# Performance work log

Measured on AMD Instinct MI355X. Metric: run time of the kernel, lower is better.

The kernel has to match this reference:

```python
import jax, jax.numpy as jnp
import numpy as np

DIM = 1024
MEM = 512
HEAD = DIM // 2


def setup_inputs() -> dict:
    key = jax.random.key(0)
    k0, k1, k2, k3, k4 = jax.random.split(key, 5)
    x = jax.random.normal(k0, (4, 8192, DIM), dtype=jnp.float32)
    keys_real = jax.random.normal(k1, (MEM, HEAD), dtype=jnp.float32) * 0.02
    keys_imag = jax.random.normal(k2, (MEM, HEAD), dtype=jnp.float32) * 0.02
    values_real = jax.random.normal(k3, (MEM, HEAD), dtype=jnp.float32) * 0.02
    values_imag = jax.random.normal(k4, (MEM, HEAD), dtype=jnp.float32) * 0.02
    return {"x": x, "keys_real": keys_real, "keys_imag": keys_imag,
            "values_real": values_real, "values_imag": values_imag}


def reference(x, keys_real, keys_imag, values_real, values_imag):
    input_shape = x.shape
    temperature = HEAD ** (-0.5)
    x_flat = x.reshape(-1, DIM)                       # [N, dim]
    q, p = jnp.split(x_flat, 2, axis=-1)              # each [N, head]
    # dual real/imag score matmuls summed -> energy [N, mem]
    energy = jnp.einsum('nh,mh->nm', q, keys_real) + jnp.einsum('nh,mh->nm', p, keys_imag)
    attn = jax.nn.softmax(energy * temperature, axis=-1)
    out_real = jnp.einsum('nm,mh->nh', attn, values_real)
    out_imag = jnp.einsum('nm,mh->nh', attn, values_imag)
    return jnp.concatenate([out_real, out_imag], axis=-1).reshape(input_shape)
```

## Files before the change

kernel.cpp:

```cpp
#include <hip/hip_runtime.h>


#define DIMX   1024
#define MEMN   512
#define NROWS  32768
#define TEMP   0.04419417382415922f

typedef __bf16 bf16;
typedef __bf16 bf16x8 __attribute__((ext_vector_type(8)));
typedef float  f32x4  __attribute__((ext_vector_type(4)));

__device__ __forceinline__ void gload_lds16(const void* g, void* l) {
    __builtin_amdgcn_global_load_lds(
        (const __attribute__((address_space(1))) unsigned*)g,
        (__attribute__((address_space(3))) unsigned*)l,
        16, 0, 0);
}
__device__ __forceinline__ void gl_b16x8(bf16x8& d, const bf16* p) {
    asm volatile("global_load_dwordx4 %0, %1, off" : "=v"(d) : "v"(p));
}
__device__ __forceinline__ void gl_f32x4(f32x4& d, const float* p) {
    asm volatile("global_load_dwordx4 %0, %1, off" : "=v"(d) : "v"(p));
}
#define VMW(N)     do { asm volatile("s_waitcnt vmcnt(" #N ")" ::: "memory"); \
                        __builtin_amdgcn_sched_barrier(0); } while (0)
#define WAITBAR(N) do { asm volatile("s_waitcnt vmcnt(" #N ") lgkmcnt(0)\n\t" \
                        "s_barrier" ::: "memory");                            \
                        __builtin_amdgcn_sched_barrier(0); } while (0)
#define VMWBAR(N)  do { asm volatile("s_waitcnt vmcnt(" #N ")\n\t"            \
                        "s_barrier" ::: "memory");                            \
                        __builtin_amdgcn_sched_barrier(0); } while (0)

__global__ __launch_bounds__(256) void pack_kv_kernel(const float* __restrict__ kr,
                                                      const float* __restrict__ ki,
                                                      const float* __restrict__ vr,
                                                      const float* __restrict__ vi,
                                                      bf16* __restrict__ Kb,
                                                      bf16* __restrict__ Vb) {
    const int idx = blockIdx.x * 256 + threadIdx.x;
    const int e = idx & 7, l = (idx >> 3) & 63;
    const int lm = l & 15, g = l >> 4;
    {
        const int t = (idx >> 9) & 31, c = idx >> 14;
        const int row = t * 16 + lm, k = c * 32 + g * 8 + e;
        const float v = (k < 512) ? kr[row * 512 + k] : ki[row * 512 + (k - 512)];
        Kb[idx] = (bf16)v;
    }
    {
        const int t = (idx >> 9) & 63, c = idx >> 15;
        const int h = t * 16 + lm, m = c * 32 + g * 8 + e;
        const float v = (h < 512) ? vr[m * 512 + h] : vi[m * 512 + (h - 512)];
        Vb[idx] = (bf16)v;
    }
}

__global__ __launch_bounds__(256, 2) void energy_softmax_kernel(
        const float* __restrict__ x,
        const bf16*  __restrict__ Kb,
        bf16* __restrict__ attn) {
    __shared__ __align__(16) bf16 Xs[2][64 * 32];
    __shared__ float red[64][4][2];

    const int tid  = threadIdx.x;
    const int wv   = tid >> 6, lane = tid & 63;
    const int lm   = lane & 15, g = lane >> 4;
    const int rowB = blockIdx.x * 64;

    const int sr = tid >> 2, sc = tid & 3;
    const float* xsrc = x + (size_t)(rowB + sr) * DIMX + sc * 8;
    const int xw_off = sr * 64 + ((sc ^ ((sr >> 1) & 3)) << 4);

    const bf16* kbase = Kb + (wv * 8) * 512 + lane * 8;

    f32x4 acc[4][8] = {};
    f32x4 xa, xb;
    bf16x8 kf0[8], kf1[8];

#define K_PREF(DST, C) { _Pragma("unroll") for (int j = 0; j < 8; ++j)         \
        gl_b16x8(DST[j], kbase + (size_t)(C) * 16384 + j * 512); }
#define X_PREF(S) { gl_f32x4(xa, xsrc + (S) * 32);                             \
                    gl_f32x4(xb, xsrc + (S) * 32 + 4); }
#define X_WR(B) { bf16x8 w;                                                    \
    w[0]=(bf16)xa[0]; w[1]=(bf16)xa[1]; w[2]=(bf16)xa[2]; w[3]=(bf16)xa[3];    \
    w[4]=(bf16)xb[0]; w[5]=(bf16)xb[1]; w[6]=(bf16)xb[2]; w[7]=(bf16)xb[3];    \
    *(bf16x8*)((char*)Xs[B] + xw_off) = w; }
#define COMPUTE_E(XB, KF) { bf16x8 af[4];                                      \
    _Pragma("unroll") for (int i = 0; i < 4; ++i) { const int r = i * 16 + lm; \
        af[i] = *(const bf16x8*)((const char*)Xs[XB] + r * 64                  \
                                 + ((g ^ ((r >> 1) & 3)) << 4)); }             \
    __builtin_amdgcn_s_setprio(1);                                             \
    _Pragma("unroll") for (int i = 0; i < 4; ++i)                              \
        _Pragma("unroll") for (int j = 0; j < 8; ++j)                          \
            acc[i][j] = __builtin_amdgcn_mfma_f32_16x16x32_bf16(               \
                af[i], KF[j], acc[i][j], 0, 0, 0);                             \
    __builtin_amdgcn_s_setprio(0); }
#define STEP_E(KCUR, KNXT, XB, CH_K, CH_X)                                     \
    K_PREF(KNXT, CH_K);                                   \
    VMW(10);                              \
    COMPUTE_E(XB, KCUR);                                                       \
    VMW(8);                                                 \
    X_WR((XB) ^ 1);                                                           \
    X_PREF(CH_X);                                         \
    WAITBAR(10);

    X_PREF(0);
    K_PREF(kf0, 0);
    VMW(8);  X_WR(0);
    X_PREF(1);
    WAITBAR(10);

    for (int t = 0; t < 30; t += 2) {
        STEP_E(kf0, kf1, 0, t + 1, t + 2);
        STEP_E(kf1, kf0, 1, t + 2, t + 3);
    }
    K_PREF(kf1, 31);
    VMW(10);
    COMPUTE_E(0, kf0);
    VMW(8);
    X_WR(1);
    WAITBAR(8);
    VMW(0);
    COMPUTE_E(1, kf1);

#undef K_PREF
#undef X_PREF
#undef X_WR
#undef COMPUTE_E
#undef STEP_E

    float fac[4][4];
    #pragma unroll
    for (int i = 0; i < 4; ++i) {
        #pragma unroll
        for (int rg = 0; rg < 4; ++rg) {
            float m = acc[i][0][rg] * TEMP;
            #pragma unroll
            for (int j = 1; j < 8; ++j) m = fmaxf(m, acc[i][j][rg] * TEMP);
            m = fmaxf(m, __shfl_xor(m, 1));
            m = fmaxf(m, __shfl_xor(m, 2));
            m = fmaxf(m, __shfl_xor(m, 4));
            m = fmaxf(m, __shfl_xor(m, 8));
            float s = 0.f;
            #pragma unroll
            for (int j = 0; j < 8; ++j) {
                const float v = __expf(acc[i][j][rg] * TEMP - m);
                acc[i][j][rg] = v;
                s += v;
            }
            s += __shfl_xor(s, 1);
            s += __shfl_xor(s, 2);
            s += __shfl_xor(s, 4);
            s += __shfl_xor(s, 8);
            const int rr = i * 16 + g * 4 + rg;
            if (lm == 0) { red[rr][wv][0] = m; red[rr][wv][1] = s; }
            fac[i][rg] = m;
        }
    }
    __syncthreads();
    #pragma unroll
    for (int i = 0; i < 4; ++i) {
        #pragma unroll
        for (int rg = 0; rg < 4; ++rg) {
            const int rr = i * 16 + g * 4 + rg;
            const float m0 = red[rr][0][0], s0 = red[rr][0][1];
            const float m1 = red[rr][1][0], s1 = red[rr][1][1];
            const float m2 = red[rr][2][0], s2 = red[rr][2][1];
            const float m3 = red[rr][3][0], s3 = red[rr][3][1];
            const float M  = fmaxf(fmaxf(m0, m1), fmaxf(m2, m3));
            const float S  = s0 * __expf(m0 - M) + s1 * __expf(m1 - M)
                           + s2 * __expf(m2 - M) + s3 * __expf(m3 - M);
            fac[i][rg] = __expf(fac[i][rg] - M) / S;
        }
    }
    #pragma unroll
    for (int i = 0; i < 4; ++i) {
        #pragma unroll
        for (int rg = 0; rg < 4; ++rg) {
            const size_t rr = (size_t)(rowB + i * 16 + g * 4 + rg);
            bf16* p = attn + rr * MEMN + wv * 128 + lm;
            const float f = fac[i][rg];
            #pragma unroll
            for (int j = 0; j < 8; ++j)
                p[j * 16] = (bf16)(acc[i][j][rg] * f);
        }
    }
}

__global__ __launch_bounds__(256, 2) void gemm2_kernel(const bf16* __restrict__ A,
                                                       const bf16* __restrict__ Vb,
                                                       float* __restrict__ C) {
    __shared__ __align__(16) bf16 As[4][128 * 32];

    const int cpx = gridDim.x >> 3;
    const int l   = ((int)blockIdx.x & 7) * cpx + ((int)blockIdx.x >> 3);
    const int bx  = l & 7, by = l >> 3;

    const int tid  = threadIdx.x;
    const int wave = tid >> 6, lane = tid & 63;
    const int lm   = lane & 15, g = lane >> 4;
    const int rowB = by * 128;
    const int wrow = (wave >> 1) * 64;

    const bf16* vbase = Vb + (bx * 8 + (wave & 1) * 4) * 512 + lane * 8;

    f32x4 acc[4][4] = {};
    bf16x8 bf0[4], bf1[4];

#define A_STAGE(BI, C0) { _Pragma("unroll") for (int li = 0; li < 2; ++li) {    \
        const int q = wave * 2 + li;                                            \
        const int r = q * 16 + (lane >> 2);                                     \
        const int ch = lane & 3;                                                \
        gload_lds16(A + (size_t)(rowB + r) * 512 + (C0) * 32                    \
                      + ((ch ^ ((r >> 1) & 3)) << 3),                           \
                    (char*)As[BI] + q * 1024); } }
#define B_PREF(DST, C0) { _Pragma("unroll") for (int j = 0; j < 4; ++j)         \
        gl_b16x8(DST[j], vbase + (size_t)(C0) * 32768 + j * 512); }
#define COMPUTE_G(BI, BF) { bf16x8 af[4];                                       \
    _Pragma("unroll") for (int i = 0; i < 4; ++i) {                             \
        const int r = wrow + i * 16 + lm;                                       \
        af[i] = *(const bf16x8*)((const char*)As[BI] + r * 64                   \
                                 + ((g ^ ((r >> 1) & 3)) << 4)); }              \
    __builtin_amdgcn_s_setprio(1);                                              \
    _Pragma("unroll") for (int i = 0; i < 4; ++i)                               \
        _Pragma("unroll") for (int j = 0; j < 4; ++j)                           \
            acc[i][j] = __builtin_amdgcn_mfma_f32_16x16x32_bf16(                \
                af[i], BF[j], acc[i][j], 0, 0, 0);                              \
    __builtin_amdgcn_s_setprio(0); }
#define STEP_G(BCUR, BNXT, T)                                                   \
    A_STAGE((T + 2) & 3, T + 2);                     \
    B_PREF(BNXT, T + 1);                                             \
    VMW(6);                             \
    VMWBAR(6);                        \
    COMPUTE_G((T) & 3, BCUR);

    A_STAGE(0, 0);
    A_STAGE(1, 1);
    B_PREF(bf0, 0);
    for (int t = 0; t < 14; t += 2) {
        STEP_G(bf0, bf1, t);
        STEP_G(bf1, bf0, t + 1);
    }
    B_PREF(bf1, 15);
    VMW(4);
    VMWBAR(4);
    COMPUTE_G(2, bf0);
    VMW(0);
    COMPUTE_G(3, bf1);

#undef A_STAGE
#undef B_PREF
#undef COMPUTE_G
#undef STEP_G

    const int r0 = rowB + wrow + g * 4;
    const int c0 = bx * 128 + (wave & 1) * 64 + lm;
    #pragma unroll
    for (int i = 0; i < 4; ++i) {
        #pragma unroll
        for (int j = 0; j < 4; ++j) {
            #pragma unroll
            for (int r = 0; r < 4; ++r)
                C[(size_t)(r0 + i * 16 + r) * DIMX + (c0 + j * 16)] = acc[i][j][r];
        }
    }
}

extern "C" void kernel_launch(void* const* d_in, const int* in_sizes, int n_in,
                              void* d_out, int out_size, void* d_ws, size_t ws_size,
                              hipStream_t stream) {
    const float* x  = (const float*)d_in[0];
    const float* kr = (const float*)d_in[1];
    const float* ki = (const float*)d_in[2];
    const float* vr = (const float*)d_in[3];
    const float* vi = (const float*)d_in[4];
    float* out = (float*)d_out;

    char* ws = (char*)d_ws;
    bf16* Kb   = (bf16*)ws;
    bf16* Vb   = (bf16*)(ws + 1048576);
    bf16* attn = (bf16*)(ws + 2097152);

    pack_kv_kernel<<<2048, 256, 0, stream>>>(kr, ki, vr, vi, Kb, Vb);
    energy_softmax_kernel<<<512, 256, 0, stream>>>(x, Kb, attn);
    gemm2_kernel<<<2048, 256, 0, stream>>>(attn, Vb, out);
}
```

Measured before the change: 291.5 us.

## Enlarge both kernels to 512-thread blocks with wider row and column tiles

The energy/softmax kernel now runs 8 waves per block over 128 rows, each wave covering 64 memory columns, so each staged X tile is reused across more keys. The cross-wave softmax reduction widens to 8 partials. The second GEMM now uses 512-thread blocks covering 128 rows by 512 output columns, with each wave owning a 64-column strip and all 128 rows, which reduces re-reads of the attention matrix. The cost is more accumulator registers per thread, which can cut occupancy, and the vmcnt waits were retuned by hand to match the new load counts.

```diff
diff --git a/kernel.cpp b/kernel.cpp
--- a/kernel.cpp
+++ b/kernel.cpp
@@ -54,29 +54,29 @@
     }
 }
 
-__global__ __launch_bounds__(256, 2) void energy_softmax_kernel(
+__global__ __launch_bounds__(512, 2) void energy_softmax_kernel(
         const float* __restrict__ x,
         const bf16*  __restrict__ Kb,
         bf16* __restrict__ attn) {
-    __shared__ __align__(16) bf16 Xs[2][64 * 32];
-    __shared__ float red[64][4][2];
+    __shared__ __align__(16) bf16 Xs[2][128 * 32];
+    __shared__ float red[128][8][2];
 
     const int tid  = threadIdx.x;
     const int wv   = tid >> 6, lane = tid & 63;
     const int lm   = lane & 15, g = lane >> 4;
-    const int rowB = blockIdx.x * 64;
+    const int rowB = blockIdx.x * 128;
 
     const int sr = tid >> 2, sc = tid & 3;
     const float* xsrc = x + (size_t)(rowB + sr) * DIMX + sc * 8;
     const int xw_off = sr * 64 + ((sc ^ ((sr >> 1) & 3)) << 4);
 
-    const bf16* kbase = Kb + (wv * 8) * 512 + lane * 8;
-
-    f32x4 acc[4][8] = {};
+    const bf16* kbase = Kb + (wv * 4) * 512 + lane * 8;
+
+    f32x4 acc[8][4] = {};
     f32x4 xa, xb;
-    bf16x8 kf0[8], kf1[8];
-
-#define K_PREF(DST, C) { _Pragma("unroll") for (int j = 0; j < 8; ++j)         \
+    bf16x8 kf0[4], kf1[4];
+
+#define K_PREF(DST, C) { _Pragma("unroll") for (int j = 0; j < 4; ++j)         \
         gl_b16x8(DST[j], kbase + (size_t)(C) * 16384 + j * 512); }
 #define X_PREF(S) { gl_f32x4(xa, xsrc + (S) * 32);                             \
                     gl_f32x4(xb, xsrc + (S) * 32 + 4); }
@@ -84,41 +84,41 @@
     w[0]=(bf16)xa[0]; w[1]=(bf16)xa[1]; w[2]=(bf16)xa[2]; w[3]=(bf16)xa[3];    \
     w[4]=(bf16)xb[0]; w[5]=(bf16)xb[1]; w[6]=(bf16)xb[2]; w[7]=(bf16)xb[3];    \
     *(bf16x8*)((char*)Xs[B] + xw_off) = w; }
-#define COMPUTE_E(XB, KF) { bf16x8 af[4];                                      \
-    _Pragma("unroll") for (int i = 0; i < 4; ++i) { const int r = i * 16 + lm; \
+#define COMPUTE_E(XB, KF) { bf16x8 af[8];                                      \
+    _Pragma("unroll") for (int i = 0; i < 8; ++i) { const int r = i * 16 + lm; \
         af[i] = *(const bf16x8*)((const char*)Xs[XB] + r * 64                  \
                                  + ((g ^ ((r >> 1) & 3)) << 4)); }             \
     __builtin_amdgcn_s_setprio(1);                                             \
-    _Pragma("unroll") for (int i = 0; i < 4; ++i)                              \
-        _Pragma("unroll") for (int j = 0; j < 8; ++j)                          \
+    _Pragma("unroll") for (int i = 0; i < 8; ++i)                              \
+        _Pragma("unroll") for (int j = 0; j < 4; ++j)                          \
             acc[i][j] = __builtin_amdgcn_mfma_f32_16x16x32_bf16(               \
                 af[i], KF[j], acc[i][j], 0, 0, 0);                             \
     __builtin_amdgcn_s_setprio(0); }
 #define STEP_E(KCUR, KNXT, XB, CH_K, CH_X)                                     \
     K_PREF(KNXT, CH_K);                                   \
-    VMW(10);                              \
+    VMW(6);                               \
     COMPUTE_E(XB, KCUR);                                                       \
-    VMW(8);                                                 \
-    X_WR((XB) ^ 1);                                                           \
-    X_PREF(CH_X);                                         \
-    WAITBAR(10);
+    VMW(4);                                                 \
+    X_WR((XB) ^ 1);                                                            \
+    X_PREF(CH_X);                                          \
+    WAITBAR(6);
 
     X_PREF(0);
     K_PREF(kf0, 0);
-    VMW(8);  X_WR(0);
+    VMW(4);  X_WR(0);
     X_PREF(1);
-    WAITBAR(10);
+    WAITBAR(6);
 
     for (int t = 0; t < 30; t += 2) {
         STEP_E(kf0, kf1, 0, t + 1, t + 2);
         STEP_E(kf1, kf0, 1, t + 2, t + 3);
     }
     K_PREF(kf1, 31);
-    VMW(10);
+    VMW(6);
     COMPUTE_E(0, kf0);
-    VMW(8);
+    VMW(4);
     X_WR(1);
-    WAITBAR(8);
+    WAITBAR(4);
     VMW(0);
     COMPUTE_E(1, kf1);
 
@@ -128,21 +128,21 @@
 #undef COMPUTE_E
 #undef STEP_E
 
-    float fac[4][4];
-    #pragma unroll
-    for (int i = 0; i < 4; ++i) {
+    float fac[8][4];
+    #pragma unroll
+    for (int i = 0; i < 8; ++i) {
         #pragma unroll
         for (int rg = 0; rg < 4; ++rg) {
             float m = acc[i][0][rg] * TEMP;
             #pragma unroll
-            for (int j = 1; j < 8; ++j) m = fmaxf(m, acc[i][j][rg] * TEMP);
+            for (int j = 1; j < 4; ++j) m = fmaxf(m, acc[i][j][rg] * TEMP);
             m = fmaxf(m, __shfl_xor(m, 1));
             m = fmaxf(m, __shfl_xor(m, 2));
             m = fmaxf(m, __shfl_xor(m, 4));
             m = fmaxf(m, __shfl_xor(m, 8));
             float s = 0.f;
             #pragma unroll
-            for (int j = 0; j < 8; ++j) {
+            for (int j = 0; j < 4; ++j) {
                 const float v = __expf(acc[i][j][rg] * TEMP - m);
                 acc[i][j][rg] = v;
                 s += v;
@@ -158,79 +158,75 @@
     }
     __syncthreads();
     #pragma unroll
-    for (int i = 0; i < 4; ++i) {
+    for (int i = 0; i < 8; ++i) {
         #pragma unroll
         for (int rg = 0; rg < 4; ++rg) {
             const int rr = i * 16 + g * 4 + rg;
-            const float m0 = red[rr][0][0], s0 = red[rr][0][1];
-            const float m1 = red[rr][1][0], s1 = red[rr][1][1];
-            const float m2 = red[rr][2][0], s2 = red[rr][2][1];
-            const float m3 = red[rr][3][0], s3 = red[rr][3][1];
-            const float M  = fmaxf(fmaxf(m0, m1), fmaxf(m2, m3));
-            const float S  = s0 * __expf(m0 - M) + s1 * __expf(m1 - M)
-                           + s2 * __expf(m2 - M) + s3 * __expf(m3 - M);
+            float M = red[rr][0][0];
+            #pragma unroll
+            for (int w = 1; w < 8; ++w) M = fmaxf(M, red[rr][w][0]);
+            float S = 0.f;
+            #pragma unroll
+            for (int w = 0; w < 8; ++w)
+                S += red[rr][w][1] * __expf(red[rr][w][0] - M);
             fac[i][rg] = __expf(fac[i][rg] - M) / S;
         }
     }
     #pragma unroll
-    for (int i = 0; i < 4; ++i) {
+    for (int i = 0; i < 8; ++i) {
         #pragma unroll
         for (int rg = 0; rg < 4; ++rg) {
             const size_t rr = (size_t)(rowB + i * 16 + g * 4 + rg);
-            bf16* p = attn + rr * MEMN + wv * 128 + lm;
+            bf16* p = attn + rr * MEMN + wv * 64 + lm;
             const float f = fac[i][rg];
             #pragma unroll
-            for (int j = 0; j < 8; ++j)
+            for (int j = 0; j < 4; ++j)
                 p[j * 16] = (bf16)(acc[i][j][rg] * f);
         }
     }
 }
 
-__global__ __launch_bounds__(256, 2) void gemm2_kernel(const bf16* __restrict__ A,
+__global__ __launch_bounds__(512, 2) void gemm2_kernel(const bf16* __restrict__ A,
                                                        const bf16* __restrict__ Vb,
                                                        float* __restrict__ C) {
     __shared__ __align__(16) bf16 As[4][128 * 32];
 
     const int cpx = gridDim.x >> 3;
     const int l   = ((int)blockIdx.x & 7) * cpx + ((int)blockIdx.x >> 3);
-    const int bx  = l & 7, by = l >> 3;
+    const int bx  = l & 1, by = l >> 1;
 
     const int tid  = threadIdx.x;
-    const int wave = tid >> 6, lane = tid & 63;
+    const int wv   = tid >> 6, lane = tid & 63;
     const int lm   = lane & 15, g = lane >> 4;
     const int rowB = by * 128;
-    const int wrow = (wave >> 1) * 64;
-
-    const bf16* vbase = Vb + (bx * 8 + (wave & 1) * 4) * 512 + lane * 8;
-
-    f32x4 acc[4][4] = {};
+
+    const int sr = tid >> 2, sc = tid & 3;
+
+    const bf16* vbase = Vb + (bx * 32 + wv * 4) * 512 + lane * 8;
+
+    f32x4 acc[8][4] = {};
     bf16x8 bf0[4], bf1[4];
 
-#define A_STAGE(BI, C0) { _Pragma("unroll") for (int li = 0; li < 2; ++li) {    \
-        const int q = wave * 2 + li;                                            \
-        const int r = q * 16 + (lane >> 2);                                     \
-        const int ch = lane & 3;                                                \
-        gload_lds16(A + (size_t)(rowB + r) * 512 + (C0) * 32                    \
-                      + ((ch ^ ((r >> 1) & 3)) << 3),                           \
-                    (char*)As[BI] + q * 1024); } }
+#define A_STAGE(BI, C0)                                                         \
+    gload_lds16(A + (size_t)(rowB + sr) * 512 + (C0) * 32                       \
+                  + ((sc ^ ((sr >> 1) & 3)) << 3),                              \
+                (char*)As[BI] + wv * 1024);
 #define B_PREF(DST, C0) { _Pragma("unroll") for (int j = 0; j < 4; ++j)         \
         gl_b16x8(DST[j], vbase + (size_t)(C0) * 32768 + j * 512); }
-#define COMPUTE_G(BI, BF) { bf16x8 af[4];                                       \
-    _Pragma("unroll") for (int i = 0; i < 4; ++i) {                             \
-        const int r = wrow + i * 16 + lm;                                       \
+#define COMPUTE_G(BI, BF) { bf16x8 af[8];                                       \
+    _Pragma("unroll") for (int i = 0; i < 8; ++i) { const int r = i * 16 + lm;  \
         af[i] = *(const bf16x8*)((const char*)As[BI] + r * 64                   \
                                  + ((g ^ ((r >> 1) & 3)) << 4)); }              \
     __builtin_amdgcn_s_setprio(1);                                              \
-    _Pragma("unroll") for (int i = 0; i < 4; ++i)                               \
+    _Pragma("unroll") for (int i = 0; i < 8; ++i)                               \
         _Pragma("unroll") for (int j = 0; j < 4; ++j)                           \
             acc[i][j] = __builtin_amdgcn_mfma_f32_16x16x32_bf16(                \
                 af[i], BF[j], acc[i][j], 0, 0, 0);                              \
     __builtin_amdgcn_s_setprio(0); }
 #define STEP_G(BCUR, BNXT, T)                                                   \
-    A_STAGE((T + 2) & 3, T + 2);                     \
-    B_PREF(BNXT, T + 1);                                             \
-    VMW(6);                             \
-    VMWBAR(6);                        \
+    A_STAGE((T + 2) & 3, T + 2);                                        \
+    B_PREF(BNXT, T + 1);                                          \
+    VMWBAR(5);                                 \
     COMPUTE_G((T) & 3, BCUR);
 
     A_STAGE(0, 0);
@@ -241,7 +237,6 @@
         STEP_G(bf1, bf0, t + 1);
     }
     B_PREF(bf1, 15);
-    VMW(4);
     VMWBAR(4);
     COMPUTE_G(2, bf0);
     VMW(0);
@@ -252,15 +247,15 @@
 #undef COMPUTE_G
 #undef STEP_G
 
-    const int r0 = rowB + wrow + g * 4;
-    const int c0 = bx * 128 + (wave & 1) * 64 + lm;
-    #pragma unroll
-    for (int i = 0; i < 4; ++i) {
+    const int c0 = bx * 512 + wv * 64 + lm;
+    #pragma unroll
+    for (int i = 0; i < 8; ++i) {
         #pragma unroll
         for (int j = 0; j < 4; ++j) {
             #pragma unroll
             for (int r = 0; r < 4; ++r)
-                C[(size_t)(r0 + i * 16 + r) * DIMX + (c0 + j * 16)] = acc[i][j][r];
+                C[(size_t)(rowB + i * 16 + g * 4 + r) * DIMX + (c0 + j * 16)]
+                    = acc[i][j][r];
         }
     }
 }
@@ -281,6 +276,6 @@
     bf16* attn = (bf16*)(ws + 2097152);
 
     pack_kv_kernel<<<2048, 256, 0, stream>>>(kr, ki, vr, vi, Kb, Vb);
-    energy_softmax_kernel<<<512, 256, 0, stream>>>(x, Kb, attn);
-    gemm2_kernel<<<2048, 256, 0, stream>>>(attn, Vb, out);
-}
+    energy_softmax_kernel<<<256, 512, 0, stream>>>(x, Kb, attn);
+    gemm2_kernel<<<512, 512, 0, stream>>>(attn, Vb, out);
+}
```

New measurement: 301.8 us. 1.04x slower.

## Double K-step per barrier period in both GEMM pipelines

Applied to the files above, without the earlier changes.

The energy kernel now stages 64-wide X chunks (two K-steps) per LDS buffer with a wider XOR swizzle, so each barrier covers two MFMA blocks. The value GEMM grows its LDS ring from 4 to 8 stages and processes two chunks per period with four B register buffers. The aim is to halve the barrier and wait count and deepen prefetch. In exchange it uses more LDS and registers, which may lower occupancy or cause spills.

```diff
diff --git a/kernel.cpp b/kernel.cpp
--- a/kernel.cpp
+++ b/kernel.cpp
@@ -58,7 +58,7 @@
         const float* __restrict__ x,
         const bf16*  __restrict__ Kb,
         bf16* __restrict__ attn) {
-    __shared__ __align__(16) bf16 Xs[2][64 * 32];
+    __shared__ __align__(16) bf16 Xs[2][64 * 64];
     __shared__ float red[64][4][2];
 
     const int tid  = threadIdx.x;
@@ -67,66 +67,75 @@
     const int rowB = blockIdx.x * 64;
 
     const int sr = tid >> 2, sc = tid & 3;
-    const float* xsrc = x + (size_t)(rowB + sr) * DIMX + sc * 8;
-    const int xw_off = sr * 64 + ((sc ^ ((sr >> 1) & 3)) << 4);
+    const float* xsrc = x + (size_t)(rowB + sr) * DIMX + sc * 16;
 
     const bf16* kbase = Kb + (wv * 8) * 512 + lane * 8;
 
     f32x4 acc[4][8] = {};
-    f32x4 xa, xb;
-    bf16x8 kf0[8], kf1[8];
+    f32x4 xa0, xa1, xa2, xa3;
+    bf16x8 kfA[8], kfB[8];
 
 #define K_PREF(DST, C) { _Pragma("unroll") for (int j = 0; j < 8; ++j)         \
         gl_b16x8(DST[j], kbase + (size_t)(C) * 16384 + j * 512); }
-#define X_PREF(S) { gl_f32x4(xa, xsrc + (S) * 32);                             \
-                    gl_f32x4(xb, xsrc + (S) * 32 + 4); }
-#define X_WR(B) { bf16x8 w;                                                    \
-    w[0]=(bf16)xa[0]; w[1]=(bf16)xa[1]; w[2]=(bf16)xa[2]; w[3]=(bf16)xa[3];    \
-    w[4]=(bf16)xb[0]; w[5]=(bf16)xb[1]; w[6]=(bf16)xb[2]; w[7]=(bf16)xb[3];    \
-    *(bf16x8*)((char*)Xs[B] + xw_off) = w; }
-#define COMPUTE_E(XB, KF) { bf16x8 af[4];                                      \
+#define X_PREF(P) { gl_f32x4(xa0, xsrc + (P) * 64);                            \
+                    gl_f32x4(xa1, xsrc + (P) * 64 + 4);                        \
+                    gl_f32x4(xa2, xsrc + (P) * 64 + 8);                        \
+                    gl_f32x4(xa3, xsrc + (P) * 64 + 12); }
+#define X_WR(B) { bf16x8 w0, w1;                                               \
+    w0[0]=(bf16)xa0[0]; w0[1]=(bf16)xa0[1]; w0[2]=(bf16)xa0[2]; w0[3]=(bf16)xa0[3]; \
+    w0[4]=(bf16)xa1[0]; w0[5]=(bf16)xa1[1]; w0[6]=(bf16)xa1[2]; w0[7]=(bf16)xa1[3]; \
+    w1[0]=(bf16)xa2[0]; w1[1]=(bf16)xa2[1]; w1[2]=(bf16)xa2[2]; w1[3]=(bf16)xa2[3]; \
+    w1[4]=(bf16)xa3[0]; w1[5]=(bf16)xa3[1]; w1[6]=(bf16)xa3[2]; w1[7]=(bf16)xa3[3]; \
+    *(bf16x8*)((char*)Xs[B] + sr * 128 + (((2 * sc)     ^ (sr & 7)) << 4)) = w0; \
+    *(bf16x8*)((char*)Xs[B] + sr * 128 + (((2 * sc + 1) ^ (sr & 7)) << 4)) = w1; }
+#define COMPUTE_E(PB, S, KF) { bf16x8 af[4];                                   \
     _Pragma("unroll") for (int i = 0; i < 4; ++i) { const int r = i * 16 + lm; \
-        af[i] = *(const bf16x8*)((const char*)Xs[XB] + r * 64                  \
-                                 + ((g ^ ((r >> 1) & 3)) << 4)); }             \
+        af[i] = *(const bf16x8*)((const char*)Xs[PB] + r * 128                 \
+                                 + (((((S) * 4) + g) ^ (r & 7)) << 4)); }      \
     __builtin_amdgcn_s_setprio(1);                                             \
     _Pragma("unroll") for (int i = 0; i < 4; ++i)                              \
         _Pragma("unroll") for (int j = 0; j < 8; ++j)                          \
             acc[i][j] = __builtin_amdgcn_mfma_f32_16x16x32_bf16(               \
                 af[i], KF[j], acc[i][j], 0, 0, 0);                             \
     __builtin_amdgcn_s_setprio(0); }
-#define STEP_E(KCUR, KNXT, XB, CH_K, CH_X)                                     \
-    K_PREF(KNXT, CH_K);                                   \
-    VMW(10);                              \
-    COMPUTE_E(XB, KCUR);                                                       \
-    VMW(8);                                                 \
-    X_WR((XB) ^ 1);                                                           \
-    X_PREF(CH_X);                                         \
-    WAITBAR(10);
 
     X_PREF(0);
-    K_PREF(kf0, 0);
-    VMW(8);  X_WR(0);
+    K_PREF(kfA, 0);
+    VMW(8);
+    X_WR(0);
     X_PREF(1);
-    WAITBAR(10);
-
-    for (int t = 0; t < 30; t += 2) {
-        STEP_E(kf0, kf1, 0, t + 1, t + 2);
-        STEP_E(kf1, kf0, 1, t + 2, t + 3);
-    }
-    K_PREF(kf1, 31);
-    VMW(10);
-    COMPUTE_E(0, kf0);
+    WAITBAR(12);
+
+    for (int p = 0; p < 14; ++p) {
+        const int pb = p & 1;
+        K_PREF(kfB, 2 * p + 1);
+        VMW(12);
+        COMPUTE_E(pb, 0, kfA);
+        K_PREF(kfA, 2 * p + 2);
+        VMW(8);
+        COMPUTE_E(pb, 1, kfB);
+        X_WR(pb ^ 1);
+        X_PREF(p + 2);
+        WAITBAR(12);
+    }
+    K_PREF(kfB, 29);
+    VMW(12);
+    COMPUTE_E(0, 0, kfA);
+    K_PREF(kfA, 30);
     VMW(8);
+    COMPUTE_E(0, 1, kfB);
     X_WR(1);
     WAITBAR(8);
+    K_PREF(kfB, 31);
+    VMW(8);
+    COMPUTE_E(1, 0, kfA);
     VMW(0);
-    COMPUTE_E(1, kf1);
+    COMPUTE_E(1, 1, kfB);
 
 #undef K_PREF
 #undef X_PREF
 #undef X_WR
 #undef COMPUTE_E
-#undef STEP_E
 
     float fac[4][4];
     #pragma unroll
@@ -189,7 +198,7 @@
 __global__ __launch_bounds__(256, 2) void gemm2_kernel(const bf16* __restrict__ A,
                                                        const bf16* __restrict__ Vb,
                                                        float* __restrict__ C) {
-    __shared__ __align__(16) bf16 As[4][128 * 32];
+    __shared__ __align__(16) bf16 As[8][128 * 32];
 
     const int cpx = gridDim.x >> 3;
     const int l   = ((int)blockIdx.x & 7) * cpx + ((int)blockIdx.x >> 3);
@@ -204,7 +213,7 @@
     const bf16* vbase = Vb + (bx * 8 + (wave & 1) * 4) * 512 + lane * 8;
 
     f32x4 acc[4][4] = {};
-    bf16x8 bf0[4], bf1[4];
+    bf16x8 bfA[4], bfB[4], bfC[4], bfD[4];
 
 #define A_STAGE(BI, C0) { _Pragma("unroll") for (int li = 0; li < 2; ++li) {    \
         const int q = wave * 2 + li;                                            \
@@ -226,31 +235,39 @@
             acc[i][j] = __builtin_amdgcn_mfma_f32_16x16x32_bf16(                \
                 af[i], BF[j], acc[i][j], 0, 0, 0);                              \
     __builtin_amdgcn_s_setprio(0); }
-#define STEP_G(BCUR, BNXT, T)                                                   \
-    A_STAGE((T + 2) & 3, T + 2);                     \
-    B_PREF(BNXT, T + 1);                                             \
-    VMW(6);                             \
-    VMWBAR(6);                        \
-    COMPUTE_G((T) & 3, BCUR);
-
-    A_STAGE(0, 0);
-    A_STAGE(1, 1);
-    B_PREF(bf0, 0);
-    for (int t = 0; t < 14; t += 2) {
-        STEP_G(bf0, bf1, t);
-        STEP_G(bf1, bf0, t + 1);
-    }
-    B_PREF(bf1, 15);
-    VMW(4);
-    VMWBAR(4);
-    COMPUTE_G(2, bf0);
+#define PERIOD_G(P, C0F, C1F, N0F, N1F)                                         \
+    B_PREF(N0F, 2 * (P) + 2);                                                   \
+    B_PREF(N1F, 2 * (P) + 3);                                        \
+    VMW(12);                                         \
+    COMPUTE_G((2 * (P)) & 7, C0F);                                              \
+    COMPUTE_G((2 * (P) + 1) & 7, C1F);                                          \
+    A_STAGE((2 * (P) + 4) & 7, 2 * (P) + 4);                                    \
+    A_STAGE((2 * (P) + 5) & 7, 2 * (P) + 5);                         \
+    VMWBAR(12);
+
+    A_STAGE(0, 0);  A_STAGE(1, 1);
+    B_PREF(bfA, 0); B_PREF(bfB, 1);
+    A_STAGE(2, 2);  A_STAGE(3, 3);
+    VMWBAR(12);
+
+    for (int p = 0; p < 6; p += 2) {
+        PERIOD_G(p,     bfA, bfB, bfC, bfD);
+        PERIOD_G(p + 1, bfC, bfD, bfA, bfB);
+    }
+    B_PREF(bfC, 14);
+    B_PREF(bfD, 15);
+    VMW(12);
+    COMPUTE_G(4, bfA);
+    COMPUTE_G(5, bfB);
+    VMWBAR(8);
     VMW(0);
-    COMPUTE_G(3, bf1);
+    COMPUTE_G(6, bfC);
+    COMPUTE_G(7, bfD);
 
 #undef A_STAGE
 #undef B_PREF
 #undef COMPUTE_G
-#undef STEP_G
+#undef PERIOD_G
 
     const int r0 = rowB + wrow + g * 4;
     const int c0 = bx * 128 + (wave & 1) * 64 + lm;
```

After: 289.4 us. About the same (-0.7%).
